# Performance work log

Measured on AMD Instinct MI355X. Metric: run time of the kernel, lower is better.

The kernel has to match this reference:

```python
import jax, jax.numpy as jnp
import numpy as np

B, T, D = 32, 2048, 80
K1 = K2 = 3
S1 = S2 = 2
CB_DIM, CB_SIZE = 512, 1024
MASK_P = 0.1
NOISE_STD = 0.1
INPUT_DIM = D * K1 * K2  # 720


def _win_idx(T_in, k, s):
    Tp = (T_in - k) // s + 1
    return jnp.arange(Tp)[:, None] * s + jnp.arange(k)[None, :]  # (Tp, k)


def _unfold(x, k, s):
    # matches torch x.unfold(1, k, s).view(B, Tp, -1): out[b, t, f*k + j] = x[b, t*s + j, f]
    idx = _win_idx(x.shape[1], k, s)
    w = x[:, idx, :]                 # (B, Tp, k, F)
    w = jnp.swapaxes(w, 2, 3)        # (B, Tp, F, k)
    return w.reshape(w.shape[0], w.shape[1], -1)


def setup_inputs() -> dict:
    key = jax.random.key(0)
    k1, k2, k3, k4, k5 = jax.random.split(key, 5)
    raw_feats = jax.random.normal(k1, (B, T, D), jnp.float32)
    auged_feats = jax.random.normal(k2, (B, T, D), jnp.float32)
    length = jax.random.randint(k3, (B,), T // 2, T + 1)
    xav = (2.0 / (INPUT_DIM + CB_DIM)) ** 0.5  # xavier_normal std
    projector = jax.random.normal(k4, (INPUT_DIM, CB_DIM), jnp.float32) * xav
    codebook = jax.random.normal(k5, (CB_SIZE, CB_DIM), jnp.float32)
    return {"raw_feats": raw_feats, "auged_feats": auged_feats, "length": length,
            "projector": projector, "codebook": codebook}


def reference(raw_feats, auged_feats, length, projector, codebook):
    T1 = (T - K1) // S1 + 1
    T2 = (T1 - K2) // S2 + 1
    idx1 = _win_idx(T, K1, S1)                         # (T1, K1)
    idx2 = _win_idx(T1, K2, S2)                        # (T2, K2)
    frame_windows = idx1[idx2].reshape(T2, K1 * K2)    # (T2, 9) original frame idx per subsampled step
    label_lengths = ((length - K1) // S1 + 1 - K2) // S2 + 1  # (B,)

    # --- label path: two torch-style unfolds -> project -> nearest codebook entry ---
    stacked = _unfold(_unfold(raw_feats, K1, S1), K2, S2)     # (B, T2, 720)
    targets = jnp.matmul(stacked, projector)                  # (B, T2, 512)
    # squared-euclidean expansion; same argmin as ||t - c||
    dist = (jnp.sum(targets * targets, axis=-1, keepdims=True)
            - 2.0 * jnp.einsum('btd,cd->btc', targets, codebook)
            + jnp.sum(codebook * codebook, axis=-1))          # (B, T2, 1024)
    labels = jnp.argmin(dist, axis=-1) + 1                    # labels start from 1; 0 = ignore idx
    valid = jnp.arange(T2)[None, :] < label_lengths[:, None]  # (B, T2)
    labels = jnp.where(valid, labels, 0)[None]                # (num_codebooks=1, B, T2)

    # --- static (span length 1) random masking on valid subsampled steps ---
    mkey = jax.random.key(42)
    km, kn = jax.random.split(mkey)
    masked = (jax.random.uniform(km, (B, T2)) < MASK_P) & valid
    masked_dim = masked.astype(jnp.float32)                   # (B, T2)
    # scatter masked subsampled steps back onto original frame indices (union of windows)
    hits = jnp.zeros((B, T), jnp.float32).at[:, frame_windows].add(masked_dim[:, :, None])
    frame_mask = hits > 0                                     # (B, T)
    noise = NOISE_STD * jax.random.normal(kn, (B, T, D), auged_feats.dtype)
    masked_feats = jnp.where(frame_mask[:, :, None], noise, auged_feats)
    return masked_feats, labels, masked_dim
```

## Files before the change

kernel.cpp:

```cpp
#include <hip/hip_runtime.h>
#include <cstdint>

#define B_    32
#define T_    2048
#define D_    80
#define T2_   511
#define NROW  16352
#define GK    720
#define CBD   512
#define CBS   1024
#define HMASK 8176
#define HN    2621440
#define NP    16384
#define KB    23

using bfrag = __attribute__((ext_vector_type(8))) short;
using f32x4 = __attribute__((ext_vector_type(4))) float;
using s4    = __attribute__((ext_vector_type(4))) short;
using s8    = __attribute__((ext_vector_type(8))) short;

__device__ inline ushort f2bf(float f){
  uint32_t u = __float_as_uint(f);
  uint32_t r = (u + 0x7FFFu + ((u >> 16) & 1u)) >> 16;
  return (ushort)r;
}
__device__ inline float bf2f(ushort h){ return __uint_as_float(((uint32_t)h) << 16); }

#define GLL16(gsrc, ldst) __builtin_amdgcn_global_load_lds( \
    (__attribute__((address_space(1))) void*)(gsrc), \
    (__attribute__((address_space(3))) void*)(ldst), 16, 0, 0)

__host__ __device__ inline uint32_t rotl_(uint32_t v, int d){ return (v<<d)|(v>>(32-d)); }

__host__ __device__ inline void tf2x32(uint32_t k0, uint32_t k1, uint32_t& x0, uint32_t& x1){
  uint32_t ks2 = k0 ^ k1 ^ 0x1BD11BDAu;
  x0 += k0; x1 += k1;
  const int r0[4] = {13,15,26,6}, r1[4] = {17,29,16,24};
#pragma unroll
  for (int i=0;i<4;i++){ x0 += x1; x1 = rotl_(x1, r0[i]); x1 ^= x0; }
  x0 += k1; x1 += ks2 + 1u;
#pragma unroll
  for (int i=0;i<4;i++){ x0 += x1; x1 = rotl_(x1, r1[i]); x1 ^= x0; }
  x0 += ks2; x1 += k0 + 2u;
#pragma unroll
  for (int i=0;i<4;i++){ x0 += x1; x1 = rotl_(x1, r0[i]); x1 ^= x0; }
  x0 += k0; x1 += k1 + 3u;
#pragma unroll
  for (int i=0;i<4;i++){ x0 += x1; x1 = rotl_(x1, r1[i]); x1 ^= x0; }
  x0 += k1; x1 += ks2 + 4u;
#pragma unroll
  for (int i=0;i<4;i++){ x0 += x1; x1 = rotl_(x1, r0[i]); x1 ^= x0; }
  x0 += ks2; x1 += k0 + 5u;
}

__device__ inline float erfinv_f(float x){
  float w = -log1pf(-x*x);
  float p;
  if (w < 5.0f){
    w -= 2.5f;
    p = 2.81022636e-08f;
    p = fmaf(p, w, 3.43273939e-07f);
    p = fmaf(p, w, -3.5233877e-06f);
    p = fmaf(p, w, -4.39150654e-06f);
    p = fmaf(p, w, 0.00021858087f);
    p = fmaf(p, w, -0.00125372503f);
    p = fmaf(p, w, -0.00417768164f);
    p = fmaf(p, w, 0.246640727f);
    p = fmaf(p, w, 1.50140941f);
  } else {
    w = sqrtf(w) - 3.0f;
    p = -0.000200214257f;
    p = fmaf(p, w, 0.000100950558f);
    p = fmaf(p, w, 0.00134934322f);
    p = fmaf(p, w, -0.00367342844f);
    p = fmaf(p, w, 0.00573950773f);
    p = fmaf(p, w, -0.0076224613f);
    p = fmaf(p, w, 0.00943887047f);
    p = fmaf(p, w, 1.00167406f);
    p = fmaf(p, w, 2.83297682f);
  }
  return p * x;
}

__device__ inline int label_len(int L){ return (((L - 3) / 2) - 2) / 2 + 1; }

__global__ void cbnorm_k(const float* __restrict__ cb, ushort* __restrict__ W0, ushort* __restrict__ W1){
  int c = blockIdx.x, lane = threadIdx.x;
  double s = 0.0;
  for (int k = lane; k < CBD; k += 64){ float v = cb[c*CBD + k]; s += (double)v * (double)v; }
#pragma unroll
  for (int off = 32; off; off >>= 1) s += __shfl_down(s, off);
  float nf = (float)s;
  nf = __shfl(nf, 0);
  size_t base = ((size_t)(KB-1)*CBS + c)*32;
  int sw = ((c >> 1) & 3) << 3;
  if (lane == 16){
    float h = -0.5f * nf;
    ushort h0 = f2bf(h); ushort h1 = f2bf(h - bf2f(h0));
    W0[base + (16 ^ sw)] = h0; W1[base + (16 ^ sw)] = h1;
  } else if (lane > 16 && lane < 32){
    W0[base + (lane ^ sw)] = 0; W1[base + (lane ^ sw)] = 0;
  }
}

__global__ void gather_k(const float* __restrict__ raw, ushort* __restrict__ S0, ushort* __restrict__ S1){
  int idx = blockIdx.x * 256 + threadIdx.x;
  int g  = idx & 3;
  int n  = (idx >> 2) & (NP - 1);
  int kb = idx >> 16;
  int b = n / T2_, t2 = n - b * T2_;
  s8 o0, o1;
#pragma unroll
  for (int j = 0; j < 8; ++j){
    int k = kb*32 + g*8 + j;
    float v = 0.f;
    if (n < NROW){
      if (k < GK){
        int d = k / 9, rem = k - 9*d;
        int k1 = rem / 3, k2 = rem - 3*k1;
        int tm = 4*t2 + 2*k2 + k1;
        v = raw[(b * T_ + tm) * D_ + d];
      } else if (k == GK) v = 1.f;
    }
    ushort h0 = f2bf(v); ushort h1 = f2bf(v - bf2f(h0));
    o0[j] = (short)h0; o1[j] = (short)h1;
  }
  int gs = g ^ ((n >> 1) & 3);
  size_t off = ((size_t)kb*NP + n)*32 + gs*8;
  *(s8*)&S0[off] = o0;
  *(s8*)&S1[off] = o1;
}

__global__ __launch_bounds__(256) void wgemm_k(const float* __restrict__ P, const float* __restrict__ cb,
                                               float* __restrict__ Wp){
  __shared__ float sP[16][68];
  __shared__ float sC[16][68];
  int r0 = blockIdx.y * 64, c0 = blockIdx.x * 64;
  int kz = blockIdx.z;
  int tid = threadIdx.x, tx = tid & 15, ty = tid >> 4;
  float acc[4][4] = {};
  for (int k0 = kz * 128; k0 < kz * 128 + 128; k0 += 16){
    __syncthreads();
    {
      int r = tid >> 2, kq = tid & 3;
      int rr = r0 + r;
      float4 v = {0.f,0.f,0.f,0.f};
      if (rr < GK) v = *(const float4*)&P[rr * CBD + k0 + kq * 4];
      sP[kq*4+0][r] = v.x; sP[kq*4+1][r] = v.y; sP[kq*4+2][r] = v.z; sP[kq*4+3][r] = v.w;
      float4 w = *(const float4*)&cb[(c0 + r) * CBD + k0 + kq * 4];
      sC[kq*4+0][r] = w.x; sC[kq*4+1][r] = w.y; sC[kq*4+2][r] = w.z; sC[kq*4+3][r] = w.w;
    }
    __syncthreads();
#pragma unroll
    for (int kk = 0; kk < 16; ++kk){
      float4 a = *(const float4*)&sP[kk][ty * 4];
      float4 b = *(const float4*)&sC[kk][tx * 4];
      float av[4] = {a.x,a.y,a.z,a.w}, bv[4] = {b.x,b.y,b.z,b.w};
#pragma unroll
      for (int i = 0; i < 4; ++i)
#pragma unroll
        for (int j = 0; j < 4; ++j) acc[i][j] = fmaf(av[i], bv[j], acc[i][j]);
    }
  }
#pragma unroll
  for (int i = 0; i < 4; ++i){
    int r = r0 + ty * 4 + i;
    if (r < GK){
      float4 o; o.x = acc[i][0]; o.y = acc[i][1]; o.z = acc[i][2]; o.w = acc[i][3];
      *(float4*)&Wp[((size_t)kz * GK + r) * CBS + c0 + tx * 4] = o;
    }
  }
}

__global__ void wreduce_k(const float* __restrict__ Wp, ushort* __restrict__ W0, ushort* __restrict__ W1){
  int idx = blockIdx.x * 256 + threadIdx.x;
  int r = idx >> 10, c = idx & (CBS - 1);
  float v = Wp[(size_t)r * CBS + c]
          + Wp[((size_t)GK + r) * CBS + c]
          + Wp[((size_t)2*GK + r) * CBS + c]
          + Wp[((size_t)3*GK + r) * CBS + c];
  ushort h0 = f2bf(v); ushort h1 = f2bf(v - bf2f(h0));
  size_t o = ((size_t)(r >> 5) * CBS + c) * 32 + ((r & 31) ^ (((c >> 1) & 3) << 3));
  W0[o] = h0; W1[o] = h1;
}

__global__ __launch_bounds__(512, 2) void score_k(const ushort* __restrict__ S0, const ushort* __restrict__ S1,
                                                  const ushort* __restrict__ W0, const ushort* __restrict__ W1,
                                                  float* __restrict__ pval, int* __restrict__ pidx){
  extern __shared__ ushort lds[];
  int tid = threadIdx.x;
  int lane = tid & 63, wid = tid >> 6;
  int wm = wid >> 2, wn = wid & 3;
  int g = lane >> 4, lr = lane & 15;
  int gsw = g ^ ((lr >> 1) & 3);

  int id = blockIdx.x;
  int xcd = id & 7, slot = id >> 3;
  int cidx = slot & 3, ridx = (xcd << 3) | (slot >> 2);
  int n0 = ridx * 256, c0 = cidx * 256;

  int p = wid >> 1, h = wid & 1;
  const ushort* src0;
  size_t kstride;
  if      (p == 0){ src0 = S0 + (size_t)n0*32; kstride = (size_t)NP*32; }
  else if (p == 1){ src0 = S1 + (size_t)n0*32; kstride = (size_t)NP*32; }
  else if (p == 2){ src0 = W0 + (size_t)c0*32; kstride = (size_t)CBS*32; }
  else            { src0 = W1 + (size_t)c0*32; kstride = (size_t)CBS*32; }
  src0 += h * 4096;

  f32x4 acc[8][4] = {};

  {
    ushort* dst = lds + (size_t)p*8192 + h*4096;
#pragma unroll
    for (int q = 0; q < 8; ++q) GLL16(src0 + q*512 + lane*8, dst + q*512);
  }
  int buf = 0;
  for (int kb = 0; kb < KB; ++kb){
    if (kb + 1 < KB){
      const ushort* s = src0 + (size_t)(kb+1)*kstride;
      ushort* dst = lds + (size_t)((buf^1)*4 + p)*8192 + h*4096;
#pragma unroll
      for (int q = 0; q < 8; ++q) GLL16(s + q*512 + lane*8, dst + q*512);
      asm volatile("s_waitcnt vmcnt(8)" ::: "memory");
    } else {
      asm volatile("s_waitcnt vmcnt(0)" ::: "memory");
    }
    __builtin_amdgcn_s_barrier();
    __builtin_amdgcn_sched_barrier(0);

    const ushort* A0 = lds + (size_t)(buf*4 + 0)*8192;
    const ushort* A1 = lds + (size_t)(buf*4 + 1)*8192;
    const ushort* B0 = lds + (size_t)(buf*4 + 2)*8192;
    const ushort* B1 = lds + (size_t)(buf*4 + 3)*8192;

    bfrag b0[4], b1[4];
#pragma unroll
    for (int nt = 0; nt < 4; ++nt){
      int off = (wn*64 + nt*16 + lr)*32 + gsw*8;
      b0[nt] = *(const bfrag*)&B0[off];
      b1[nt] = *(const bfrag*)&B1[off];
    }
#pragma unroll
    for (int hf = 0; hf < 2; ++hf){
      bfrag a0[4], a1[4];
#pragma unroll
      for (int mtl = 0; mtl < 4; ++mtl){
        int off = (wm*128 + (hf*4 + mtl)*16 + lr)*32 + gsw*8;
        a0[mtl] = *(const bfrag*)&A0[off];
        a1[mtl] = *(const bfrag*)&A1[off];
      }
      __builtin_amdgcn_s_setprio(1);
#pragma unroll
      for (int mtl = 0; mtl < 4; ++mtl)
#pragma unroll
        for (int nt = 0; nt < 4; ++nt)
          acc[hf*4+mtl][nt] = __builtin_amdgcn_mfma_f32_16x16x32_bf16(a0[mtl], b0[nt], acc[hf*4+mtl][nt], 0,0,0);
#pragma unroll
      for (int mtl = 0; mtl < 4; ++mtl)
#pragma unroll
        for (int nt = 0; nt < 4; ++nt)
          acc[hf*4+mtl][nt] = __builtin_amdgcn_mfma_f32_16x16x32_bf16(a0[mtl], b1[nt], acc[hf*4+mtl][nt], 0,0,0);
#pragma unroll
      for (int mtl = 0; mtl < 4; ++mtl)
#pragma unroll
        for (int nt = 0; nt < 4; ++nt)
          acc[hf*4+mtl][nt] = __builtin_amdgcn_mfma_f32_16x16x32_bf16(a1[mtl], b0[nt], acc[hf*4+mtl][nt], 0,0,0);
      __builtin_amdgcn_s_setprio(0);
    }
    __builtin_amdgcn_sched_barrier(0);
    __builtin_amdgcn_s_barrier();
    buf ^= 1;
  }

#pragma unroll
  for (int mt = 0; mt < 8; ++mt){
    float bv[4]; int bi[4];
#pragma unroll
    for (int r = 0; r < 4; ++r){
      float best = 3.4e38f; int besti = 0;
#pragma unroll
      for (int nt = 0; nt < 4; ++nt){
        float d = -2.f * acc[mt][nt][r];
        int c = c0 + wn*64 + nt*16 + lr;
        if (d < best){ best = d; besti = c; }
      }
      bv[r] = best; bi[r] = besti;
    }
#pragma unroll
    for (int off = 1; off < 16; off <<= 1){
#pragma unroll
      for (int r = 0; r < 4; ++r){
        float ov = __shfl_xor(bv[r], off);
        int   oi = __shfl_xor(bi[r], off);
        if (ov < bv[r] || (ov == bv[r] && oi < bi[r])){ bv[r] = ov; bi[r] = oi; }
      }
    }
    if (lr == 0){
      int pp = cidx*4 + wn;
#pragma unroll
      for (int r = 0; r < 4; ++r){
        int n = n0 + wm*128 + mt*16 + g*4 + r;
        pval[(size_t)pp*NP + n] = bv[r];
        pidx[(size_t)pp*NP + n] = bi[r];
      }
    }
  }
}

__global__ void combine_k(const float* __restrict__ pval, const int* __restrict__ pidx,
                          const int* __restrict__ len, float* __restrict__ lb){
  int n = blockIdx.x * 256 + threadIdx.x;
  if (n >= NROW) return;
  float bv = pval[n]; int bi = pidx[n];
#pragma unroll
  for (int p = 1; p < 16; ++p){
    float v = pval[(size_t)p*NP + n]; int ii = pidx[(size_t)p*NP + n];
    if (v < bv || (v == bv && ii < bi)){ bv = v; bi = ii; }
  }
  int b = n / T2_, t2 = n - b * T2_;
  lb[n] = (t2 < label_len(len[b])) ? (float)(bi + 1) : 0.f;
}

__device__ inline void emit_mask(const int* len, float* md, int i, uint32_t bits){
  float u = __uint_as_float((bits >> 9) | 0x3F800000u) - 1.0f;
  int b = i / T2_, t2 = i - b * T2_;
  bool m = (u < 0.1f) && (t2 < label_len(len[b]));
  md[i] = m ? 1.0f : 0.0f;
}

__global__ void mask_k(const int* __restrict__ len, float* __restrict__ md, uint32_t km0, uint32_t km1){
  int j = blockIdx.x * 256 + threadIdx.x;
  if (j >= HMASK) return;
  uint32_t x0 = (uint32_t)j, x1 = (uint32_t)(j + HMASK);
  tf2x32(km0, km1, x0, x1);
  emit_mask(len, md, j, x0);
  emit_mask(len, md, j + HMASK, x1);
}

__device__ inline bool frame_masked(const float* md, int i){
  int tabs = i / D_;
  int t = tabs & (T_ - 1);
  int b = i / (D_ * T_);
  int lo = (t < 3) ? 0 : ((t - 3) >> 2);
  int hi = t >> 2; if (hi > T2_ - 1) hi = T2_ - 1;
  bool m = false;
  for (int t2 = lo; t2 <= hi; ++t2) m = m || (md[b * T2_ + t2] != 0.f);
  return m;
}

__device__ inline float noise_from_bits(uint32_t bits){
  float f = __uint_as_float((bits >> 9) | 0x3F800000u) - 1.0f;
  const float LOV = -0.99999994f;
  float u = fmaf(f, 2.0f, LOV);
  u = fmaxf(LOV, u);
  return 0.1f * (1.41421356f * erfinv_f(u));
}

__global__ void feats_k(const float* __restrict__ aug, const float* __restrict__ md,
                        float* __restrict__ mf, uint32_t kn0, uint32_t kn1){
  int j = blockIdx.x * 256 + threadIdx.x;
  bool m1 = frame_masked(md, j);
  bool m2 = frame_masked(md, j + HN);
  if (m1 || m2){
    uint32_t x0 = (uint32_t)j, x1 = (uint32_t)(j + HN);
    tf2x32(kn0, kn1, x0, x1);
    mf[j]      = m1 ? noise_from_bits(x0) : aug[j];
    mf[j + HN] = m2 ? noise_from_bits(x1) : aug[j + HN];
  } else {
    mf[j]      = aug[j];
    mf[j + HN] = aug[j + HN];
  }
}

extern "C" void kernel_launch(void* const* d_in, const int* in_sizes, int n_in,
                              void* d_out, int out_size, void* d_ws, size_t ws_size,
                              hipStream_t stream){
  const float* raw  = (const float*)d_in[0];
  const float* aug  = (const float*)d_in[1];
  const int*   len  = (const int*)  d_in[2];
  const float* proj = (const float*)d_in[3];
  const float* cb   = (const float*)d_in[4];

  float* out = (float*)d_out;
  float* mf  = out;
  float* lb  = out + 5242880;
  float* md  = out + 5259232;

  ushort* w  = (ushort*)d_ws;
  ushort* W0 = w;
  ushort* W1 = W0 + (size_t)KB*CBS*32;
  ushort* S0 = W1 + (size_t)KB*CBS*32;
  ushort* S1 = S0 + (size_t)KB*NP*32;
  float* pval = (float*)(S1 + (size_t)KB*NP*32);
  int*   pidx = (int*)(pval + (size_t)16*NP);
  float* Wp   = (float*)(pidx + (size_t)16*NP);

  hipFuncSetAttribute((const void*)score_k, hipFuncAttributeMaxDynamicSharedMemorySize, 131072);

  uint32_t a0 = 0u, a1 = 2u, b0 = 1u, b1 = 3u;
  tf2x32(0u, 42u, a0, a1);
  tf2x32(0u, 42u, b0, b1);
  uint32_t km0 = a0, km1 = b0, kn0 = a1, kn1 = b1;

  cbnorm_k<<<CBS, 64, 0, stream>>>(cb, W0, W1);
  wgemm_k<<<dim3(CBS / 64, 12, 4), 256, 0, stream>>>(proj, cb, Wp);
  wreduce_k<<<(GK * CBS) / 256, 256, 0, stream>>>(Wp, W0, W1);
  gather_k<<<(KB * NP * 4) / 256, 256, 0, stream>>>(raw, S0, S1);
  score_k<<<256, 512, 131072, stream>>>(S0, S1, W0, W1, pval, pidx);
  combine_k<<<(NROW + 255) / 256, 256, 0, stream>>>(pval, pidx, len, lb);
  mask_k<<<(HMASK + 255) / 256, 256, 0, stream>>>(len, md, km0, km1);
  feats_k<<<HN / 256, 256, 0, stream>>>(aug, md, mf, kn0, kn1);
}
```

Before: 151.8 us.

## Load codebook fragments directly from global and fuse combine into mask kernel

The score GEMM no longer stages the codebook (W0/W1) tiles through LDS. Each wave reads its B fragments straight from global/L2 into registers, and only the activation tiles (S0/S1) stay double-buffered in a 64KB static LDS array. This halves LDS use and load traffic per block, at the cost of exposed global-load latency on the B operand and a full vmcnt(0) wait every iteration. The combine kernel is also merged into the mask kernel to remove one launch.

```diff
diff --git a/kernel.cpp b/kernel.cpp
--- a/kernel.cpp
+++ b/kernel.cpp
@@ -16,7 +16,6 @@
 
 using bfrag = __attribute__((ext_vector_type(8))) short;
 using f32x4 = __attribute__((ext_vector_type(4))) float;
-using s4    = __attribute__((ext_vector_type(4))) short;
 using s8    = __attribute__((ext_vector_type(8))) short;
 
 __device__ inline ushort f2bf(float f){
@@ -185,9 +184,9 @@
 }
 
 __global__ __launch_bounds__(512, 2) void score_k(const ushort* __restrict__ S0, const ushort* __restrict__ S1,
-                                                  const ushort* __restrict__ W0, const ushort* __restrict__ W1,
+                                                  const ushort* __restrict__ W0g, const ushort* __restrict__ W1g,
                                                   float* __restrict__ pval, int* __restrict__ pidx){
-  extern __shared__ ushort lds[];
+  __shared__ __align__(16) ushort lds[2 * 16384];
   int tid = threadIdx.x;
   int lane = tid & 63, wid = tid >> 6;
   int wm = wid >> 2, wn = wid & 3;
@@ -199,78 +198,70 @@
   int cidx = slot & 3, ridx = (xcd << 3) | (slot >> 2);
   int n0 = ridx * 256, c0 = cidx * 256;
 
-  int p = wid >> 1, h = wid & 1;
-  const ushort* src0;
-  size_t kstride;
-  if      (p == 0){ src0 = S0 + (size_t)n0*32; kstride = (size_t)NP*32; }
-  else if (p == 1){ src0 = S1 + (size_t)n0*32; kstride = (size_t)NP*32; }
-  else if (p == 2){ src0 = W0 + (size_t)c0*32; kstride = (size_t)CBS*32; }
-  else            { src0 = W1 + (size_t)c0*32; kstride = (size_t)CBS*32; }
-  src0 += h * 4096;
+  const ushort* sbase = (wid < 4) ? (S0 + (size_t)n0*32) : (S1 + (size_t)n0*32);
+  int ckbase  = (wid & 3) * 4;
+  int dstbase = ((wid < 4) ? 0 : 8192) + ckbase * 512;
+
+  size_t wofs0 = ((size_t)c0 + wn*64 + lr) * 32 + gsw * 8;
 
   f32x4 acc[8][4] = {};
 
-  {
-    ushort* dst = lds + (size_t)p*8192 + h*4096;
-#pragma unroll
-    for (int q = 0; q < 8; ++q) GLL16(src0 + q*512 + lane*8, dst + q*512);
-  }
-  int buf = 0;
+#pragma unroll
+  for (int q = 0; q < 4; ++q)
+    GLL16(sbase + (size_t)(ckbase + q)*512 + lane*8, lds + dstbase + q*512);
+  asm volatile("s_waitcnt vmcnt(0)" ::: "memory");
+  __builtin_amdgcn_s_barrier();
+
   for (int kb = 0; kb < KB; ++kb){
+    const ushort* cur = lds + ((kb & 1) ? 16384 : 0);
+    ushort*       nxt = lds + ((kb & 1) ? 0 : 16384);
+
+    bfrag b0c[4], b1c[4];
+    {
+      size_t wo = (size_t)kb * CBS * 32 + wofs0;
+#pragma unroll
+      for (int nt = 0; nt < 4; ++nt){
+        b0c[nt] = *(const bfrag*)&W0g[wo + (size_t)nt*512];
+        b1c[nt] = *(const bfrag*)&W1g[wo + (size_t)nt*512];
+      }
+    }
     if (kb + 1 < KB){
-      const ushort* s = src0 + (size_t)(kb+1)*kstride;
-      ushort* dst = lds + (size_t)((buf^1)*4 + p)*8192 + h*4096;
-#pragma unroll
-      for (int q = 0; q < 8; ++q) GLL16(s + q*512 + lane*8, dst + q*512);
-      asm volatile("s_waitcnt vmcnt(8)" ::: "memory");
-    } else {
-      asm volatile("s_waitcnt vmcnt(0)" ::: "memory");
-    }
+      const ushort* s = sbase + (size_t)(kb+1)*NP*32;
+#pragma unroll
+      for (int q = 0; q < 4; ++q)
+        GLL16(s + (size_t)(ckbase + q)*512 + lane*8, nxt + dstbase + q*512);
+    }
+    bfrag a0[8], a1[8];
+    {
+      int abase = (wm*128 + lr)*32 + gsw*8;
+#pragma unroll
+      for (int mt = 0; mt < 8; ++mt){
+        a0[mt] = *(const bfrag*)&cur[abase + mt*512];
+        a1[mt] = *(const bfrag*)&cur[8192 + abase + mt*512];
+      }
+    }
+#pragma unroll
+    for (int hf = 0; hf < 2; ++hf){
+      __builtin_amdgcn_s_setprio(1);
+#pragma unroll
+      for (int mtl = 0; mtl < 4; ++mtl)
+#pragma unroll
+        for (int nt = 0; nt < 4; ++nt)
+          acc[hf*4+mtl][nt] = __builtin_amdgcn_mfma_f32_16x16x32_bf16(a0[hf*4+mtl], b0c[nt], acc[hf*4+mtl][nt], 0,0,0);
+#pragma unroll
+      for (int mtl = 0; mtl < 4; ++mtl)
+#pragma unroll
+        for (int nt = 0; nt < 4; ++nt)
+          acc[hf*4+mtl][nt] = __builtin_amdgcn_mfma_f32_16x16x32_bf16(a0[hf*4+mtl], b1c[nt], acc[hf*4+mtl][nt], 0,0,0);
+#pragma unroll
+      for (int mtl = 0; mtl < 4; ++mtl)
+#pragma unroll
+        for (int nt = 0; nt < 4; ++nt)
+          acc[hf*4+mtl][nt] = __builtin_amdgcn_mfma_f32_16x16x32_bf16(a1[hf*4+mtl], b0c[nt], acc[hf*4+mtl][nt], 0,0,0);
+      __builtin_amdgcn_s_setprio(0);
+    }
+    asm volatile("s_waitcnt vmcnt(0)" ::: "memory");
     __builtin_amdgcn_s_barrier();
-    __builtin_amdgcn_sched_barrier(0);
-
-    const ushort* A0 = lds + (size_t)(buf*4 + 0)*8192;
-    const ushort* A1 = lds + (size_t)(buf*4 + 1)*8192;
-    const ushort* B0 = lds + (size_t)(buf*4 + 2)*8192;
-    const ushort* B1 = lds + (size_t)(buf*4 + 3)*8192;
-
-    bfrag b0[4], b1[4];
-#pragma unroll
-    for (int nt = 0; nt < 4; ++nt){
-      int off = (wn*64 + nt*16 + lr)*32 + gsw*8;
-      b0[nt] = *(const bfrag*)&B0[off];
-      b1[nt] = *(const bfrag*)&B1[off];
-    }
-#pragma unroll
-    for (int hf = 0; hf < 2; ++hf){
-      bfrag a0[4], a1[4];
-#pragma unroll
-      for (int mtl = 0; mtl < 4; ++mtl){
-        int off = (wm*128 + (hf*4 + mtl)*16 + lr)*32 + gsw*8;
-        a0[mtl] = *(const bfrag*)&A0[off];
-        a1[mtl] = *(const bfrag*)&A1[off];
-      }
-      __builtin_amdgcn_s_setprio(1);
-#pragma unroll
-      for (int mtl = 0; mtl < 4; ++mtl)
-#pragma unroll
-        for (int nt = 0; nt < 4; ++nt)
-          acc[hf*4+mtl][nt] = __builtin_amdgcn_mfma_f32_16x16x32_bf16(a0[mtl], b0[nt], acc[hf*4+mtl][nt], 0,0,0);
-#pragma unroll
-      for (int mtl = 0; mtl < 4; ++mtl)
-#pragma unroll
-        for (int nt = 0; nt < 4; ++nt)
-          acc[hf*4+mtl][nt] = __builtin_amdgcn_mfma_f32_16x16x32_bf16(a0[mtl], b1[nt], acc[hf*4+mtl][nt], 0,0,0);
-#pragma unroll
-      for (int mtl = 0; mtl < 4; ++mtl)
-#pragma unroll
-        for (int nt = 0; nt < 4; ++nt)
-          acc[hf*4+mtl][nt] = __builtin_amdgcn_mfma_f32_16x16x32_bf16(a1[mtl], b0[nt], acc[hf*4+mtl][nt], 0,0,0);
-      __builtin_amdgcn_s_setprio(0);
-    }
-    __builtin_amdgcn_sched_barrier(0);
-    __builtin_amdgcn_s_barrier();
-    buf ^= 1;
   }
 
 #pragma unroll
@@ -308,20 +299,6 @@
   }
 }
 
-__global__ void combine_k(const float* __restrict__ pval, const int* __restrict__ pidx,
-                          const int* __restrict__ len, float* __restrict__ lb){
-  int n = blockIdx.x * 256 + threadIdx.x;
-  if (n >= NROW) return;
-  float bv = pval[n]; int bi = pidx[n];
-#pragma unroll
-  for (int p = 1; p < 16; ++p){
-    float v = pval[(size_t)p*NP + n]; int ii = pidx[(size_t)p*NP + n];
-    if (v < bv || (v == bv && ii < bi)){ bv = v; bi = ii; }
-  }
-  int b = n / T2_, t2 = n - b * T2_;
-  lb[n] = (t2 < label_len(len[b])) ? (float)(bi + 1) : 0.f;
-}
-
 __device__ inline void emit_mask(const int* len, float* md, int i, uint32_t bits){
   float u = __uint_as_float((bits >> 9) | 0x3F800000u) - 1.0f;
   int b = i / T2_, t2 = i - b * T2_;
@@ -329,13 +306,29 @@
   md[i] = m ? 1.0f : 0.0f;
 }
 
-__global__ void mask_k(const int* __restrict__ len, float* __restrict__ md, uint32_t km0, uint32_t km1){
+__device__ inline void comb_one(const float* __restrict__ pval, const int* __restrict__ pidx,
+                                const int* __restrict__ len, float* __restrict__ lb, int n){
+  float bv = pval[n]; int bi = pidx[n];
+#pragma unroll
+  for (int p = 1; p < 16; ++p){
+    float v = pval[(size_t)p*NP + n]; int ii = pidx[(size_t)p*NP + n];
+    if (v < bv || (v == bv && ii < bi)){ bv = v; bi = ii; }
+  }
+  int b = n / T2_, t2 = n - b * T2_;
+  lb[n] = (t2 < label_len(len[b])) ? (float)(bi + 1) : 0.f;
+}
+
+__global__ void maskcomb_k(const float* __restrict__ pval, const int* __restrict__ pidx,
+                           const int* __restrict__ len, float* __restrict__ lb,
+                           float* __restrict__ md, uint32_t km0, uint32_t km1){
   int j = blockIdx.x * 256 + threadIdx.x;
   if (j >= HMASK) return;
   uint32_t x0 = (uint32_t)j, x1 = (uint32_t)(j + HMASK);
   tf2x32(km0, km1, x0, x1);
   emit_mask(len, md, j, x0);
   emit_mask(len, md, j + HMASK, x1);
+  comb_one(pval, pidx, len, lb, j);
+  comb_one(pval, pidx, len, lb, j + HMASK);
 }
 
 __device__ inline bool frame_masked(const float* md, int i){
@@ -396,8 +389,6 @@
   int*   pidx = (int*)(pval + (size_t)16*NP);
   float* Wp   = (float*)(pidx + (size_t)16*NP);
 
-  hipFuncSetAttribute((const void*)score_k, hipFuncAttributeMaxDynamicSharedMemorySize, 131072);
-
   uint32_t a0 = 0u, a1 = 2u, b0 = 1u, b1 = 3u;
   tf2x32(0u, 42u, a0, a1);
   tf2x32(0u, 42u, b0, b1);
@@ -407,8 +398,7 @@
   wgemm_k<<<dim3(CBS / 64, 12, 4), 256, 0, stream>>>(proj, cb, Wp);
   wreduce_k<<<(GK * CBS) / 256, 256, 0, stream>>>(Wp, W0, W1);
   gather_k<<<(KB * NP * 4) / 256, 256, 0, stream>>>(raw, S0, S1);
-  score_k<<<256, 512, 131072, stream>>>(S0, S1, W0, W1, pval, pidx);
-  combine_k<<<(NROW + 255) / 256, 256, 0, stream>>>(pval, pidx, len, lb);
-  mask_k<<<(HMASK + 255) / 256, 256, 0, stream>>>(len, md, km0, km1);
+  score_k<<<256, 512, 0, stream>>>(S0, S1, W0, W1, pval, pidx);
+  maskcomb_k<<<(HMASK + 255) / 256, 256, 0, stream>>>(pval, pidx, len, lb, md, km0, km1);
   feats_k<<<HN / 256, 256, 0, stream>>>(aug, md, mf, kn0, kn1);
 }
```

Measured after the change: 161.5 us. 1.06x slower.
